# Performance work log

Hardware: AMD Instinct MI355X
Metric: run time of the kernel (lower is better)

Reference implementation:

```python
import jax, jax.numpy as jnp
import numpy as np

D = 512      # embeddings_dim (in_features == out_features)
H = 4        # num_heads
MID = 2048   # mid_features
B, S = 4, 2048
EPS = 1e-5


def _ln(x, g, b):
    mu = jnp.mean(x, axis=-1, keepdims=True)
    var = jnp.mean(jnp.square(x - mu), axis=-1, keepdims=True)
    return g * (x - mu) / jnp.sqrt(var + EPS) + b


def setup_inputs() -> dict:
    key = jax.random.key(0)
    ks = jax.random.split(key, 16)
    w = 0.02  # weight init scale
    return {
        "x_encoder": jax.random.normal(ks[0], (B, S, D), jnp.float32),
        "x_decoder": jax.random.normal(ks[1], (B, S, D), jnp.float32),
        # per-head full-width projections (each head is a D->D Linear)
        "Wq": jax.random.normal(ks[2], (H, D, D), jnp.float32) * w,
        "bq": jnp.zeros((H, D), jnp.float32),
        "Wk": jax.random.normal(ks[3], (H, D, D), jnp.float32) * w,
        "bk": jnp.zeros((H, D), jnp.float32),
        "Wv": jax.random.normal(ks[4], (H, D, D), jnp.float32) * w,
        "bv": jnp.zeros((H, D), jnp.float32),
        # out_reshaper: Rearrange('b h s d -> b s (d h)') then Linear(D*H -> D)
        "Wo": jax.random.normal(ks[5], (D * H, D), jnp.float32) * w,
        "bo": jnp.zeros((D,), jnp.float32),
        "ln1_g": jnp.ones((D,), jnp.float32), "ln1_b": jnp.zeros((D,), jnp.float32),
        "ln2_g": jnp.ones((D,), jnp.float32), "ln2_b": jnp.zeros((D,), jnp.float32),
        # FouriFeedForward: D -> MID -> D with SELU
        "W1": jax.random.normal(ks[6], (D, MID), jnp.float32) * w,
        "b1": jnp.zeros((MID,), jnp.float32),
        "W2": jax.random.normal(ks[7], (MID, D), jnp.float32) * w,
        "b2": jnp.zeros((D,), jnp.float32),
        "ln3_g": jnp.ones((D,), jnp.float32), "ln3_b": jnp.zeros((D,), jnp.float32),
    }


def reference(x_encoder, x_decoder, Wq, bq, Wk, bk, Wv, bv, Wo, bo,
              ln1_g, ln1_b, ln2_g, ln2_b, W1, b1, W2, b2, ln3_g, ln3_b):
    # Fourier token mixing: per-batch fftn over (seq, feature) dims, keep real part
    xf = jnp.fft.fftn(x_decoder, axes=(1, 2)).real
    xd = _ln(x_decoder + xf, ln1_g, ln1_b)  # [B,S,D]

    # Linear multi-head attention: q from decoder, k/v from encoder.
    # qs/ks/vs: [B,H,S,D]; softmax over the HEAD axis (dim=1 in torch)
    qs = jax.nn.softmax(jnp.einsum('bsd,hde->bhse', xd, Wq) + bq[None, :, None, :], axis=1)
    ks = jax.nn.softmax(jnp.einsum('bsd,hde->bhse', x_encoder, Wk) + bk[None, :, None, :], axis=1)
    vs = jnp.einsum('bsd,hde->bhse', x_encoder, Wv) + bv[None, :, None, :]

    gc = jnp.einsum('bhsd,bhse->bhde', ks, vs)       # [B,H,D,D] global contexts
    out = jnp.einsum('bhsd,bhde->bhse', qs, gc)      # [B,H,S,D]

    # Rearrange 'b h s d -> b s (d h)': d is the slow axis, h the fast axis
    b, h, s, d = out.shape
    out = out.transpose(0, 2, 3, 1).reshape(b, s, d * h)
    attn = out @ Wo + bo                              # [B,S,D]

    x = _ln(xd + attn, ln2_g, ln2_b)
    ff = jax.nn.selu(x @ W1 + b1) @ W2 + b2           # dropout_p=0 (eval)
    x = _ln(x + ff, ln3_g, ln3_b)
    return x
```

## Files before the change

kernel.cpp:

```cpp
#include <hip/hip_runtime.h>
#include <stdint.h>

typedef __bf16 bf16;
typedef __bf16 bf16x8 __attribute__((ext_vector_type(8)));
typedef float f32x4 __attribute__((ext_vector_type(4)));

static __device__ __forceinline__ void async16(const void* g, void* l) {
  __builtin_amdgcn_global_load_lds(
      (__attribute__((address_space(1))) void*)g,
      (__attribute__((address_space(3))) void*)l, 16, 0, 0);
}

__global__ void __launch_bounds__(256) prep_all(
    const float* __restrict__ xdec, const float* __restrict__ xenc,
    bf16* __restrict__ Ttrig, bf16* __restrict__ Atrig2,
    bf16* __restrict__ xdec_b, bf16* __restrict__ xenc_b,
    const float* __restrict__ Wq, const float* __restrict__ Wk,
    const float* __restrict__ Wv, const float* __restrict__ Wo,
    const float* __restrict__ W1, const float* __restrict__ W2,
    bf16* __restrict__ BtQ, bf16* __restrict__ BtK, bf16* __restrict__ BtV,
    bf16* __restrict__ WoTh, bf16* __restrict__ W1T, bf16* __restrict__ W2T) {
  __shared__ bf16 tile[32][33];
  int id = blockIdx.x;
  if (id < 2048) {
    int idx = id * 256 + threadIdx.x;
    int d = idx & 511, jp = idx >> 9;
    int jj = jp >> 1, p = jp & 1;
    int t = (d * jj) & 511;
    float ang = (float)t * (6.283185307179586f / 512.0f);
    Ttrig[idx] = (bf16)(p ? __sinf(ang) : __cosf(ang));
  } else if (id < 11840) {
    int idx = (id - 2048) * 256 + threadIdx.x;
    int k = idx % 1088;
    int rr = idx / 1088;
    int r = rr % 1152, half = rr / 1152;
    float v = 0.0f;
    int tt = (r * k) & 2047;
    float ang = (float)tt * (6.283185307179586f / 2048.0f);
    if (half == 0) { if (r <= 1024 && k <= 1024) v = __cosf(ang); }
    else           { if (r <= 1023 && k >= 1 && k <= 1023) v = -__sinf(ang); }
    Atrig2[idx] = (bf16)v;
  } else if (id < 28224) {
    int i = (id - 11840) * 256 + threadIdx.x;
    xdec_b[i] = (bf16)xdec[i];
  } else if (id < 44608) {
    int i = (id - 28224) * 256 + threadIdx.x;
    xenc_b[i] = (bf16)xenc[i];
  } else {
    int id2 = id - 44608;
    int kind = id2 >> 10, t = id2 & 1023;
    const float* in; bf16* out; int R, C, rt, ct;
    bool iperm = false, hsel = false; int hh = 0;
    if (kind == 0)      { in = Wq; out = BtQ; R = 2048; C = 512; rt = t >> 4; ct = t & 15; iperm = true; }
    else if (kind == 1) { in = Wk; out = BtK; R = 2048; C = 512; rt = t >> 4; ct = t & 15; iperm = true; }
    else if (kind == 2) { in = Wv; out = BtV; R = 2048; C = 512; rt = t >> 4; ct = t & 15; iperm = true; }
    else if (kind == 3) {
      int zz = t >> 8, tt = t & 255;
      in = Wo; out = WoTh + (long)zz * 262144;
      R = 512; C = 512; rt = tt >> 4; ct = tt & 15; hsel = true; hh = zz;
    }
    else if (kind == 4) { in = W1; out = W1T; R = 512; C = 2048; rt = t >> 6; ct = t & 63; }
    else                { in = W2; out = W2T; R = 2048; C = 512; rt = t >> 4; ct = t & 15; }
    int c0 = ct * 32, r0 = rt * 32;
    int tx = threadIdx.x & 31, ty = threadIdx.x >> 5;
#pragma unroll
    for (int i = 0; i < 32; i += 8) {
      int r = r0 + ty + i;
      int rr = hsel ? (4 * r + hh) : r;
      tile[ty + i][tx] = (bf16)in[(long)rr * C + (c0 + tx)];
    }
    __syncthreads();
#pragma unroll
    for (int i = 0; i < 32; i += 8) {
      int cc = c0 + ty + i, rr = r0 + tx;
      if (iperm)
        out[((long)(4 * cc + (rr >> 9)) << 9) + (rr & 511)] = tile[tx][ty + i];
      else
        out[(long)cc * R + rr] = tile[tx][ty + i];
    }
  }
}

__global__ void __launch_bounds__(256) fold_y(const bf16* __restrict__ Yt,
                                              bf16* __restrict__ Yf2) {
  int idx = blockIdx.x * 256 + threadIdx.x;
  int k = idx % 1088;
  int rr = idx / 1088;
  int j = rr & 511, z = rr >> 9;
  int b = z & 3, half = z >> 2;
  const bf16* yin = Yt + (long)b * 2097152 + (long)j * 4096;
  float v = 0.0f;
  if (half == 0) {
    if (k == 0) v = (float)yin[0];
    else if (k == 1024) v = (float)yin[1024];
    else if (k < 1024) v = (float)yin[k] + (float)yin[2048 - k];
  } else {
    if (k >= 1 && k <= 1023) v = (float)yin[2048 + k] - (float)yin[4096 - k];
  }
  Yf2[(long)z * 557056 + (long)j * 1088 + k] = (bf16)v;
}

__global__ void __launch_bounds__(256) ln1_kernel(
    const float* __restrict__ xdec, const bf16* __restrict__ CSb,
    const float* __restrict__ g, const float* __restrict__ be,
    bf16* __restrict__ outb) {
  const int row = blockIdx.x, t = threadIdx.x;
  const int b = row >> 11, s = row & 2047;
  const int sp = (s <= 1024) ? s : 2048 - s;
  const float sgn = (s <= 1024) ? 1.0f : -1.0f;
  const bf16* Crow = CSb + ((long)b * 1152 + sp) * 512;
  const bf16* Srow = CSb + ((long)(b + 4) * 1152 + sp) * 512;
  const long base = (long)row * 512;
  float v0 = xdec[base + t] + (float)Crow[t] + sgn * (float)Srow[t];
  float v1 = xdec[base + t + 256] + (float)Crow[t + 256] + sgn * (float)Srow[t + 256];
  float sm = v0 + v1, q = v0 * v0 + v1 * v1;
#pragma unroll
  for (int off = 32; off > 0; off >>= 1) {
    sm += __shfl_down(sm, off);
    q += __shfl_down(q, off);
  }
  __shared__ float red[8];
  const int wv = t >> 6, ln = t & 63;
  if (ln == 0) { red[wv] = sm; red[wv + 4] = q; }
  __syncthreads();
  float S = red[0] + red[1] + red[2] + red[3];
  float Q = red[4] + red[5] + red[6] + red[7];
  float mu = S * (1.0f / 512.0f);
  float var = Q * (1.0f / 512.0f) - mu * mu;
  float rstd = rsqrtf(var + 1e-5f);
  outb[base + t] = (bf16)(g[t] * (v0 - mu) * rstd + be[t]);
  outb[base + t + 256] = (bf16)(g[t + 256] * (v1 - mu) * rstd + be[t + 256]);
}

__global__ void __launch_bounds__(256) softmax_kv(
    const bf16* __restrict__ klog, bf16* __restrict__ ksT,
    const bf16* __restrict__ vlog, bf16* __restrict__ vsT) {
  __shared__ bf16 lds[4 * 64 * 64];
  const int bid = blockIdx.x, t = threadIdx.x;
  const bool isK = bid < 1024;
  int tb = isK ? bid : (bid - 1024);
  const bf16* src = isK ? klog : vlog;
  bf16* dst = isK ? ksT : vsT;
  int b = tb >> 8, rem = tb & 255;
  int s0 = (rem >> 3) << 6, e0 = (rem & 7) << 6;
  int te = t & 63, tr = t >> 6;
#pragma unroll
  for (int i = 0; i < 16; ++i) {
    int s = tr + (i << 2);
    bf16 raw[4] __attribute__((aligned(8)));
    *(uint2*)raw = *(const uint2*)(src + ((long)(b * 2048 + s0 + s) * 2048 + 4 * (e0 + te)));
    float x0 = (float)raw[0], x1 = (float)raw[1], x2 = (float)raw[2], x3 = (float)raw[3];
    if (isK) {
      float m = fmaxf(fmaxf(x0, x1), fmaxf(x2, x3));
      float y0 = __expf(x0 - m), y1 = __expf(x1 - m), y2 = __expf(x2 - m), y3 = __expf(x3 - m);
      float rs = 1.0f / (y0 + y1 + y2 + y3);
      x0 = y0 * rs; x1 = y1 * rs; x2 = y2 * rs; x3 = y3 * rs;
    }
    int cp = ((((s >> 2) ^ (te & 15)) << 2) | (s & 3));
    int base = te * 64 + cp;
    lds[base] = (bf16)x0;
    lds[4096 + base] = (bf16)x1;
    lds[8192 + base] = (bf16)x2;
    lds[12288 + base] = (bf16)x3;
  }
  __syncthreads();
  int sc = t & 15, r = t >> 4;
#pragma unroll
  for (int i = 0; i < 16; ++i) {
    int he = r + (i << 4);
    int h = he >> 6, e = he & 63;
    int cp = (sc ^ (e & 15)) << 2;
    bf16 tmp[4] __attribute__((aligned(8)));
    *(uint2*)tmp = *(const uint2*)&lds[h * 4096 + e * 64 + cp];
    *(uint2*)(dst + ((long)(b * 4 + h) * 512 + e0 + e) * 2048 + s0 + (sc << 2)) =
        *(const uint2*)tmp;
  }
}

template <typename TA, typename TB, int WRITE_BF16, int WRITE_F32>
__global__ void __launch_bounds__(256) ln_kernel(
    const TA* __restrict__ A, const TB* __restrict__ Bv,
    const float* __restrict__ g, const float* __restrict__ be,
    bf16* __restrict__ outb, float* __restrict__ outf) {
  const int row = blockIdx.x, t = threadIdx.x;
  const long base = (long)row * 512;
  float v0 = (float)A[base + t] + (float)Bv[base + t];
  float v1 = (float)A[base + t + 256] + (float)Bv[base + t + 256];
  float s = v0 + v1, q = v0 * v0 + v1 * v1;
#pragma unroll
  for (int off = 32; off > 0; off >>= 1) {
    s += __shfl_down(s, off);
    q += __shfl_down(q, off);
  }
  __shared__ float red[8];
  const int wv = t >> 6, ln = t & 63;
  if (ln == 0) { red[wv] = s; red[wv + 4] = q; }
  __syncthreads();
  float S = red[0] + red[1] + red[2] + red[3];
  float Q = red[4] + red[5] + red[6] + red[7];
  float mu = S * (1.0f / 512.0f);
  float var = Q * (1.0f / 512.0f) - mu * mu;
  float rstd = rsqrtf(var + 1e-5f);
  float o0 = g[t] * (v0 - mu) * rstd + be[t];
  float o1 = g[t + 256] * (v1 - mu) * rstd + be[t + 256];
  if (WRITE_BF16) { outb[base + t] = (bf16)o0; outb[base + t + 256] = (bf16)o1; }
  if (WRITE_F32)  { outf[base + t] = o0; outf[base + t + 256] = o1; }
}

template <int BN, int ADDR_MODE, int HAS_BIAS, int DO_SELU, int F32OUT, int SWIZ,
          int AHEAD = 0>
__global__ void __launch_bounds__(256, 2) gemm_bt(
    const bf16* __restrict__ A, const bf16* __restrict__ Bt,
    const float* __restrict__ bias, void* __restrict__ Cout,
    int N, int K, long sAz, long sBz, long sBiasz, long sCz,
    int gx, int gy, int gin) {
  __shared__ __align__(16) bf16 lA[128 * 64];
  __shared__ __align__(16) bf16 lB[BN * 64];
  int x, y, z;
  {
    int id = blockIdx.x;
    if (SWIZ == 0) {
      x = id % gx; int t2 = id / gx; y = t2 % gy; z = t2 / gy;
    } else {
      int xcd = id & 7, r = id >> 3;
      int inner = r % gin, G = xcd + 8 * (r / gin);
      if (SWIZ == 1)      { y = G; x = inner % gx; z = inner / gx; }
      else if (SWIZ == 2) { z = G; x = inner % gx; y = inner / gx; }
      else                { x = G; y = inner % gy; z = inner / gy; }
    }
  }
  A  += (AHEAD == 1) ? sAz * (z & 3) : (AHEAD == 2) ? sAz * (z >> 2) : sAz * z;
  Bt += sBz * z;
  const int m0 = y * 128, n0 = x * BN;
  const int t = threadIdx.x;
  const int lane = t & 63, wave = t >> 6;
  const int srow = t >> 3;
  const int pch  = t & 7;
  const int lch  = pch ^ (srow & 7);
  const bf16* Ag = A  + (long)(m0 + srow) * K + lch * 8;
  const bf16* Bg = Bt + (long)(n0 + srow) * K + lch * 8;
  bf16* lAp = lA + srow * 64 + pch * 8;
  bf16* lBp = lB + srow * 64 + pch * 8;
  constexpr int MI = (BN == 128) ? 4 : 2;
  const int wm = (BN == 128) ? (wave >> 1) * 64 : wave * 32;
  const int wn = (BN == 128) ? (wave & 1) * 64 : 0;
  const int fr = lane & 15, fq = lane >> 4;

  f32x4 acc[MI][4] = {};

  for (int k0 = 0; k0 < K; k0 += 64) {
    __syncthreads();
#pragma unroll
    for (int i = 0; i < 4; ++i)
      async16(Ag + k0 + (long)(32 * i) * K, lAp + 32 * i * 64);
#pragma unroll
    for (int i = 0; i < BN / 32; ++i)
      async16(Bg + k0 + (long)(32 * i) * K, lBp + 32 * i * 64);
    __syncthreads();
#pragma unroll
    for (int kk = 0; kk < 2; ++kk) {
      bf16x8 av[MI], bfrag[4];
#pragma unroll
      for (int mi = 0; mi < MI; ++mi) {
        int r = wm + mi * 16 + fr;
        int c = (kk * 4 + fq) ^ (r & 7);
        av[mi] = *(const bf16x8*)&lA[r * 64 + c * 8];
      }
#pragma unroll
      for (int ni = 0; ni < 4; ++ni) {
        int r = wn + ni * 16 + fr;
        int c = (kk * 4 + fq) ^ (r & 7);
        bfrag[ni] = *(const bf16x8*)&lB[r * 64 + c * 8];
      }
#pragma unroll
      for (int mi = 0; mi < MI; ++mi)
#pragma unroll
        for (int ni = 0; ni < 4; ++ni)
          acc[mi][ni] = __builtin_amdgcn_mfma_f32_16x16x32_bf16(
              av[mi], bfrag[ni], acc[mi][ni], 0, 0, 0);
    }
  }

#pragma unroll
  for (int mi = 0; mi < MI; ++mi) {
#pragma unroll
    for (int ni = 0; ni < 4; ++ni) {
      const int col = n0 + wn + ni * 16 + fr;
      float bias_v = 0.0f;
      if (HAS_BIAS == 1) bias_v = bias[sBiasz * z + col];
      if (ADDR_MODE == 7) {
        const int b = z >> 2, h = z & 3;
#pragma unroll
        for (int r = 0; r < 4; ++r) {
          const int row = m0 + wm + mi * 16 + fq * 4 + r;
          ((bf16*)Cout)[((long)(b * 512 + row)) * 2048 + h * 512 + col] =
              (bf16)(acc[mi][ni][r] + bias_v);
        }
      } else if (ADDR_MODE == 8) {
        const int b = z >> 2, h = z & 3;
#pragma unroll
        for (int r = 0; r < 4; ++r) {
          const int row = m0 + wm + mi * 16 + fq * 4 + r;
          ((bf16*)Cout)[((long)(b * 512 + row)) * 2048 + 4 * col + h] =
              (bf16)(acc[mi][ni][r] + bias_v);
        }
      } else {
#pragma unroll
        for (int r = 0; r < 4; ++r) {
          const int row = m0 + wm + mi * 16 + fq * 4 + r;
          float v = acc[mi][ni][r] + bias_v;
          if (DO_SELU) v = v > 0.0f ? 1.0507009873554805f * v
                                    : 1.7580993408473766f * (__expf(v) - 1.0f);
          long addr = sCz * z + (long)row * N + col;
          if (F32OUT) ((float*)Cout)[addr] = v;
          else        ((bf16*)Cout)[addr] = (bf16)v;
        }
      }
    }
  }
}

__global__ void __launch_bounds__(256, 2) gemm_qkv(
    const bf16* __restrict__ Aq, const bf16* __restrict__ Aenc,
    const bf16* __restrict__ BQ, const bf16* __restrict__ BK,
    const bf16* __restrict__ BV,
    const float* __restrict__ bq, const float* __restrict__ bk,
    const float* __restrict__ bv,
    bf16* __restrict__ qs2, bf16* __restrict__ klog, bf16* __restrict__ vlog) {
  __shared__ __align__(16) bf16 lA[128 * 64];
  __shared__ __align__(16) bf16 lB[128 * 64];
  const int id = blockIdx.x;
  const int seg = id >> 10, sid = id & 1023;
  const int xcd = sid & 7, r = sid >> 3;
  const int x = r & 15, y = xcd + 8 * (r >> 4);
  const bf16 *A, *Bt; bf16* out; const float* bias;
  if (seg == 0)      { A = Aq;   Bt = BQ; out = qs2;  bias = bq; }
  else if (seg == 1) { A = Aenc; Bt = BK; out = klog; bias = bk; }
  else               { A = Aenc; Bt = BV; out = vlog; bias = bv; }
  const int K = 512;
  const int m0 = y * 128, n0 = x * 128;
  const int t = threadIdx.x;
  const int lane = t & 63, wave = t >> 6;
  const int srow = t >> 3, pch = t & 7, lch = pch ^ (srow & 7);
  const bf16* Ag = A  + (long)(m0 + srow) * K + lch * 8;
  const bf16* Bg = Bt + (long)(n0 + srow) * K + lch * 8;
  bf16* lAp = lA + srow * 64 + pch * 8;
  bf16* lBp = lB + srow * 64 + pch * 8;
  const int wm = (wave >> 1) * 64, wn = (wave & 1) * 64;
  const int fr = lane & 15, fq = lane >> 4;

  f32x4 acc[4][4] = {};
  for (int k0 = 0; k0 < K; k0 += 64) {
    __syncthreads();
#pragma unroll
    for (int i = 0; i < 4; ++i) {
      async16(Ag + k0 + (long)(32 * i) * K, lAp + 32 * i * 64);
      async16(Bg + k0 + (long)(32 * i) * K, lBp + 32 * i * 64);
    }
    __syncthreads();
#pragma unroll
    for (int kk = 0; kk < 2; ++kk) {
      bf16x8 av[4], bfrag[4];
#pragma unroll
      for (int mi = 0; mi < 4; ++mi) {
        int rr = wm + mi * 16 + fr;
        int c = (kk * 4 + fq) ^ (rr & 7);
        av[mi] = *(const bf16x8*)&lA[rr * 64 + c * 8];
      }
#pragma unroll
      for (int ni = 0; ni < 4; ++ni) {
        int rr = wn + ni * 16 + fr;
        int c = (kk * 4 + fq) ^ (rr & 7);
        bfrag[ni] = *(const bf16x8*)&lB[rr * 64 + c * 8];
      }
#pragma unroll
      for (int mi = 0; mi < 4; ++mi)
#pragma unroll
        for (int ni = 0; ni < 4; ++ni)
          acc[mi][ni] = __builtin_amdgcn_mfma_f32_16x16x32_bf16(
              av[mi], bfrag[ni], acc[mi][ni], 0, 0, 0);
    }
  }

  const bool do_sm = (seg == 0);
#pragma unroll
  for (int mi = 0; mi < 4; ++mi) {
#pragma unroll
    for (int ni = 0; ni < 4; ++ni) {
      const int col = n0 + wn + ni * 16 + fr;
      const float bias_v = bias[(col & 3) * 512 + (col >> 2)];
#pragma unroll
      for (int r = 0; r < 4; ++r) {
        const int row = m0 + wm + mi * 16 + fq * 4 + r;
        float v = acc[mi][ni][r] + bias_v;
        if (do_sm) {
          float m = fmaxf(v, __shfl_xor(v, 1));
          m = fmaxf(m, __shfl_xor(m, 2));
          float p = __expf(v - m);
          float s = p + __shfl_xor(p, 1);
          s += __shfl_xor(s, 2);
          v = p / s;
        }
        out[(long)row * 2048 + col] = (bf16)v;
      }
    }
  }
}

extern "C" void kernel_launch(void* const* d_in, const int* in_sizes, int n_in,
                              void* d_out, int out_size, void* d_ws, size_t ws_size,
                              hipStream_t stream) {
  (void)in_sizes; (void)n_in; (void)out_size; (void)ws_size;
  const float* x_enc = (const float*)d_in[0];
  const float* x_dec = (const float*)d_in[1];
  const float* Wq = (const float*)d_in[2];
  const float* bq = (const float*)d_in[3];
  const float* Wk = (const float*)d_in[4];
  const float* bk = (const float*)d_in[5];
  const float* Wv = (const float*)d_in[6];
  const float* bv = (const float*)d_in[7];
  const float* Wo = (const float*)d_in[8];
  const float* bo = (const float*)d_in[9];
  const float* g1 = (const float*)d_in[10];
  const float* be1 = (const float*)d_in[11];
  const float* g2 = (const float*)d_in[12];
  const float* be2 = (const float*)d_in[13];
  const float* W1 = (const float*)d_in[14];
  const float* b1 = (const float*)d_in[15];
  const float* W2 = (const float*)d_in[16];
  const float* b2 = (const float*)d_in[17];
  const float* g3 = (const float*)d_in[18];
  const float* be3 = (const float*)d_in[19];

  char* ws = (char*)d_ws;
  const size_t MB = 1u << 20;
  bf16*  midb   = (bf16*) (ws + 0);
  bf16*  klog   = (bf16*) (ws + 32 * MB);
  bf16*  attn_b = (bf16*) (ws + 32 * MB);
  bf16*  vlog   = (bf16*) (ws + 64 * MB);
  bf16*  gc     = (bf16*) (ws + 64 * MB);
  bf16*  ff_b   = (bf16*) (ws + 72 * MB);
  bf16*  Atrig2 = (bf16*) (ws + 96 * MB);
  bf16*  Ttrig  = (bf16*) (ws + 101 * MB);
  bf16*  CSb    = (bf16*) (ws + 102 * MB);
  bf16*  qs2    = (bf16*) (ws + 96 * MB);
  bf16*  xenc_b = (bf16*) (ws + 128 * MB);
  bf16*  BtQ    = (bf16*) (ws + 136 * MB);
  bf16*  BtK    = (bf16*) (ws + 138 * MB);
  bf16*  BtV    = (bf16*) (ws + 140 * MB);
  bf16*  ksT    = (bf16*) (ws + 128 * MB);
  bf16*  vsT    = (bf16*) (ws + 160 * MB);
  bf16*  xd_b   = (bf16*) (ws + 192 * MB);
  bf16*  x2_b   = (bf16*) (ws + 200 * MB);
  bf16*  gwT    = (bf16*) (ws + 208 * MB);
  bf16*  Yt     = (bf16*) (ws + 216 * MB);
  bf16*  Yf2    = (bf16*) (ws + 232 * MB);
  bf16*  WoTh   = (bf16*) (ws + 241 * MB);
  bf16*  W1T    = (bf16*) (ws + 243 * MB);
  bf16*  W2T    = (bf16*) (ws + 245 * MB);
  bf16*  xdec_b = (bf16*) (ws + 247 * MB);

  prep_all<<<50752, 256, 0, stream>>>(x_dec, x_enc, Ttrig, Atrig2, xdec_b, xenc_b,
                                      Wq, Wk, Wv, Wo, W1, W2,
                                      BtQ, BtK, BtV, WoTh, W1T, W2T);

  gemm_bt<128, 0, 0, 0, 0, 3><<<512, 256, 0, stream>>>(
      Ttrig, xdec_b, nullptr, Yt, 2048, 512, 0L, 1048576L, 0L, 2097152L, 16, 8, 32);
  fold_y<<<17408, 256, 0, stream>>>(Yt, Yf2);
  gemm_bt<64, 0, 0, 0, 0, 2, 2><<<576, 256, 0, stream>>>(
      Atrig2, Yf2, nullptr, CSb, 512, 1088, 1253376L, 557056L, 0L, 589824L, 8, 9, 72);
  ln1_kernel<<<8192, 256, 0, stream>>>(x_dec, CSb, g1, be1, xd_b);

  gemm_qkv<<<3072, 256, 0, stream>>>(xd_b, xenc_b, BtQ, BtK, BtV,
                                     bq, bk, bv, qs2, klog, vlog);
  softmax_kv<<<2048, 256, 0, stream>>>(klog, ksT, vlog, vsT);
  gemm_bt<64, 0, 0, 0, 0, 2><<<512, 256, 0, stream>>>(
      ksT, vsT, nullptr, gc, 512, 2048, 1048576L, 1048576L, 0L, 262144L, 8, 4, 32);
  gemm_bt<64, 8, 0, 0, 0, 2, 1><<<512, 256, 0, stream>>>(
      WoTh, gc, nullptr, gwT, 512, 512, 262144L, 262144L, 0L, 0L, 8, 4, 32);
  gemm_bt<64, 0, 1, 0, 0, 1><<<512, 256, 0, stream>>>(
      qs2, gwT, bo, attn_b, 512, 2048, 4194304L, 1048576L, 0L, 1048576L, 8, 16, 32);
  ln_kernel<bf16, bf16, 1, 0><<<8192, 256, 0, stream>>>(
      xd_b, attn_b, g2, be2, x2_b, nullptr);

  gemm_bt<128, 0, 1, 1, 0, 1><<<1024, 256, 0, stream>>>(
      x2_b, W1T, b1, midb, 2048, 512, 0L, 0L, 0L, 0L, 16, 64, 16);
  gemm_bt<64, 0, 1, 0, 0, 1><<<512, 256, 0, stream>>>(
      midb, W2T, b2, ff_b, 512, 2048, 0L, 0L, 0L, 0L, 8, 64, 8);
  ln_kernel<bf16, bf16, 0, 1><<<8192, 256, 0, stream>>>(
      x2_b, ff_b, g3, be3, nullptr, (float*)d_out);
}
```

Measured before the change: 412.9 us.

## Reorder Q projection columns so head softmax stays within a lane

Changes the column permutation of the Q weight matrix so that each 16-lane MFMA fragment group holds one feature across all four heads in registers (ni index), instead of interleaving heads across adjacent lanes. The head-axis softmax in the QKV epilogue then runs in registers without cross-lane shuffles and with one reciprocal per group. The consumer gwT layout (ADDR_MODE 9) is permuted to match, so the downstream qs2·gwT GEMM contraction is still consistent. Output stores become 16-element strided per lane group rather than contiguous per column, which may change write coalescing.

```diff
diff --git a/kernel.cpp b/kernel.cpp
--- a/kernel.cpp
+++ b/kernel.cpp
@@ -50,8 +50,8 @@
     int id2 = id - 44608;
     int kind = id2 >> 10, t = id2 & 1023;
     const float* in; bf16* out; int R, C, rt, ct;
-    bool iperm = false, hsel = false; int hh = 0;
-    if (kind == 0)      { in = Wq; out = BtQ; R = 2048; C = 512; rt = t >> 4; ct = t & 15; iperm = true; }
+    bool iperm = false, qperm = false, hsel = false; int hh = 0;
+    if (kind == 0)      { in = Wq; out = BtQ; R = 2048; C = 512; rt = t >> 4; ct = t & 15; iperm = true; qperm = true; }
     else if (kind == 1) { in = Wk; out = BtK; R = 2048; C = 512; rt = t >> 4; ct = t & 15; iperm = true; }
     else if (kind == 2) { in = Wv; out = BtV; R = 2048; C = 512; rt = t >> 4; ct = t & 15; iperm = true; }
     else if (kind == 3) {
@@ -73,10 +73,13 @@
 #pragma unroll
     for (int i = 0; i < 32; i += 8) {
       int cc = c0 + ty + i, rr = r0 + tx;
-      if (iperm)
-        out[((long)(4 * cc + (rr >> 9)) << 9) + (rr & 511)] = tile[tx][ty + i];
-      else
+      if (iperm) {
+        int e = cc, h = rr >> 9;
+        int n = qperm ? ((e & 15) | (h << 4) | ((e >> 4) << 6)) : (4 * e + h);
+        out[((long)n << 9) + (rr & 511)] = tile[tx][ty + i];
+      } else {
         out[(long)cc * R + rr] = tile[tx][ty + i];
+      }
     }
   }
 }
@@ -296,12 +299,13 @@
           ((bf16*)Cout)[((long)(b * 512 + row)) * 2048 + h * 512 + col] =
               (bf16)(acc[mi][ni][r] + bias_v);
         }
-      } else if (ADDR_MODE == 8) {
+      } else if (ADDR_MODE == 9) {
         const int b = z >> 2, h = z & 3;
+        const int kidx = (col & 15) | (h << 4) | ((col >> 4) << 6);
 #pragma unroll
         for (int r = 0; r < 4; ++r) {
           const int row = m0 + wm + mi * 16 + fq * 4 + r;
-          ((bf16*)Cout)[((long)(b * 512 + row)) * 2048 + 4 * col + h] =
+          ((bf16*)Cout)[((long)(b * 512 + row)) * 2048 + kidx] =
               (bf16)(acc[mi][ni][r] + bias_v);
         }
       } else {
@@ -382,26 +386,42 @@
     }
   }
 
-  const bool do_sm = (seg == 0);
-#pragma unroll
-  for (int mi = 0; mi < 4; ++mi) {
-#pragma unroll
-    for (int ni = 0; ni < 4; ++ni) {
-      const int col = n0 + wn + ni * 16 + fr;
-      const float bias_v = bias[(col & 3) * 512 + (col >> 2)];
+  if (seg == 0) {
+    const int ebase = fr + 16 * ((n0 + wn) >> 6);
+    const float b0 = bias[ebase], b1 = bias[512 + ebase],
+                b2 = bias[1024 + ebase], b3 = bias[1536 + ebase];
+#pragma unroll
+    for (int mi = 0; mi < 4; ++mi) {
 #pragma unroll
       for (int r = 0; r < 4; ++r) {
         const int row = m0 + wm + mi * 16 + fq * 4 + r;
-        float v = acc[mi][ni][r] + bias_v;
-        if (do_sm) {
-          float m = fmaxf(v, __shfl_xor(v, 1));
-          m = fmaxf(m, __shfl_xor(m, 2));
-          float p = __expf(v - m);
-          float s = p + __shfl_xor(p, 1);
-          s += __shfl_xor(s, 2);
-          v = p / s;
+        float v0 = acc[mi][0][r] + b0;
+        float v1 = acc[mi][1][r] + b1;
+        float v2 = acc[mi][2][r] + b2;
+        float v3 = acc[mi][3][r] + b3;
+        float m = fmaxf(fmaxf(v0, v1), fmaxf(v2, v3));
+        float p0 = __expf(v0 - m), p1 = __expf(v1 - m),
+              p2 = __expf(v2 - m), p3 = __expf(v3 - m);
+        float rs = 1.0f / (p0 + p1 + p2 + p3);
+        const long ob = (long)row * 2048 + n0 + wn + fr;
+        out[ob]      = (bf16)(p0 * rs);
+        out[ob + 16] = (bf16)(p1 * rs);
+        out[ob + 32] = (bf16)(p2 * rs);
+        out[ob + 48] = (bf16)(p3 * rs);
+      }
+    }
+  } else {
+#pragma unroll
+    for (int mi = 0; mi < 4; ++mi) {
+#pragma unroll
+      for (int ni = 0; ni < 4; ++ni) {
+        const int col = n0 + wn + ni * 16 + fr;
+        const float bias_v = bias[(col & 3) * 512 + (col >> 2)];
+#pragma unroll
+        for (int r = 0; r < 4; ++r) {
+          const int row = m0 + wm + mi * 16 + fq * 4 + r;
+          out[(long)row * 2048 + col] = (bf16)(acc[mi][ni][r] + bias_v);
         }
-        out[(long)row * 2048 + col] = (bf16)v;
       }
     }
   }
@@ -476,7 +496,7 @@
   softmax_kv<<<2048, 256, 0, stream>>>(klog, ksT, vlog, vsT);
   gemm_bt<64, 0, 0, 0, 0, 2><<<512, 256, 0, stream>>>(
       ksT, vsT, nullptr, gc, 512, 2048, 1048576L, 1048576L, 0L, 262144L, 8, 4, 32);
-  gemm_bt<64, 8, 0, 0, 0, 2, 1><<<512, 256, 0, stream>>>(
+  gemm_bt<64, 9, 0, 0, 0, 2, 1><<<512, 256, 0, stream>>>(
       WoTh, gc, nullptr, gwT, 512, 512, 262144L, 262144L, 0L, 0L, 8, 4, 32);
   gemm_bt<64, 0, 1, 0, 0, 1><<<512, 256, 0, stream>>>(
       qs2, gwT, bo, attn_b, 512, 2048, 4194304L, 1048576L, 0L, 1048576L, 8, 16, 32);
```

After: 406.9 us. About the same (-1.4%).
